# Kernel tuning notes

Hardware: AMD Instinct MI355X
Metric: run time of the kernel (lower is better)

The kernel has to match this reference:

```python
import jax, jax.numpy as jnp
import numpy as np

EMBED_DIM = 1024
N_HEADS = 16
HEAD_DIM = EMBED_DIM // N_HEADS


def setup_inputs() -> dict:
    key = jax.random.key(0)
    k_x, k_wi, k_bi, k_wo, k_bo = jax.random.split(key, 5)
    B, N, C = 4, 2048, EMBED_DIM
    scale = 1.0 / np.sqrt(C)
    return {
        "x": jax.random.normal(k_x, (B, N, C), dtype=jnp.float32),
        "w_in": jax.random.normal(k_wi, (C, 3 * C), dtype=jnp.float32) * scale,
        "b_in": jax.random.normal(k_bi, (3 * C,), dtype=jnp.float32) * 0.01,
        "w_out": jax.random.normal(k_wo, (C, C), dtype=jnp.float32) * scale,
        "b_out": jax.random.normal(k_bo, (C,), dtype=jnp.float32) * 0.01,
    }


def reference(x, w_in, b_in, w_out, b_out):
    B, N, C = x.shape
    H, D = N_HEADS, HEAD_DIM
    qkv = x @ w_in + b_in  # (B, N, 3C)
    q, k, v = jnp.split(qkv, 3, axis=-1)
    # (B, H, N, D)
    q = q.reshape(B, N, H, D).transpose(0, 2, 1, 3)
    k = k.reshape(B, N, H, D).transpose(0, 2, 1, 3)
    v = v.reshape(B, N, H, D).transpose(0, 2, 1, 3)
    # Naive attention: full (B,H,N,N) scores, NO sqrt(d) scaling (as in source)
    scores = jnp.einsum("bhnd,bhmd->bhnm", q, k)
    attn = jax.nn.softmax(scores, axis=-1)
    out = jnp.einsum("bhnm,bhmd->bhnd", attn, v)
    out = out.transpose(0, 2, 1, 3).reshape(B, N, C)
    return out @ w_out + b_out
```

## Files before the change

kernel.cpp:

```cpp
#include <hip/hip_runtime.h>
#include <hip/hip_bf16.h>
#include <stdint.h>

typedef __attribute__((ext_vector_type(8))) __bf16 bf8v;
typedef __attribute__((ext_vector_type(4))) float f4v;

#define L2E 1.44269504088896f

__device__ __forceinline__ unsigned short f2bf(float f) {
  union { float f; unsigned u; } v; v.f = f;
  unsigned r = v.u + 0x7fffu + ((v.u >> 16) & 1u);
  return (unsigned short)(r >> 16);
}

__device__ __forceinline__ unsigned pk2bf(float f0, float f1) {
  union { __hip_bfloat162 h; unsigned u; } c;
  c.h = __float22bfloat162_rn(make_float2(f0, f1));
  return c.u;
}

__device__ __forceinline__ float exp2_hw(float x) {
  return __builtin_amdgcn_exp2f(x);
}

__device__ __forceinline__ void gl_lds16(const void* g, void* l) {
  __builtin_amdgcn_global_load_lds(
      (__attribute__((address_space(1))) void*)(g),
      (__attribute__((address_space(3))) void*)(l), 16, 0, 0);
}

__global__ void cast_bf16_kernel(const float* __restrict__ in,
                                 unsigned short* __restrict__ out) {
  int i = blockIdx.x * 256 + threadIdx.x;
  float4 v = ((const float4*)in)[i];
  ushort4 o;
  o.x = f2bf(v.x); o.y = f2bf(v.y); o.z = f2bf(v.z); o.w = f2bf(v.w);
  ((ushort4*)out)[i] = o;
}

__global__ void transpose_w_kernel(const float* __restrict__ w_in,
                                   const float* __restrict__ w_out,
                                   unsigned short* __restrict__ wiT,
                                   unsigned short* __restrict__ woT) {
  __shared__ float tile[32][33];
  int bx = blockIdx.x;
  const float* in; unsigned short* out; int C, c0;
  if (bx < 96) { in = w_in;  out = wiT; C = 3072; c0 = bx * 32; }
  else         { in = w_out; out = woT; C = 1024; c0 = (bx - 96) * 32; }
  int r0 = blockIdx.y * 32;
  int tx = threadIdx.x, ty = threadIdx.y;
#pragma unroll
  for (int j = 0; j < 4; ++j)
    tile[ty + 8 * j][tx] = in[(size_t)(r0 + ty + 8 * j) * C + c0 + tx];
  __syncthreads();
#pragma unroll
  for (int j = 0; j < 4; ++j)
    out[(size_t)(c0 + ty + 8 * j) * 1024 + r0 + tx] = f2bf(tile[tx][ty + 8 * j]);
}

__global__ void transpose_v_kernel(const unsigned short* __restrict__ qkv,
                                   unsigned short* __restrict__ vtg) {
  __shared__ unsigned short tile[32][33];
  int bh = blockIdx.z;
  int d0 = blockIdx.y * 32;
  int n0 = blockIdx.x * 32;
  int b = bh >> 4, h = bh & 15;
  int tx = threadIdx.x, ty = threadIdx.y;
  const unsigned short* src = qkv + (size_t)b * 2048 * 3072 + 2048 + h * 64 + d0;
#pragma unroll
  for (int j = 0; j < 4; ++j)
    tile[ty + 8 * j][tx] = src[(size_t)(n0 + ty + 8 * j) * 3072 + tx];
  __syncthreads();
  unsigned short* dst = vtg + ((size_t)bh * 64) * 2048;
#pragma unroll
  for (int j = 0; j < 4; ++j)
    dst[(size_t)(d0 + ty + 8 * j) * 2048 + n0 + tx] = tile[tx][ty + 8 * j];
}

__global__ __launch_bounds__(256, 2) void gemm_bt(
    const unsigned short* __restrict__ A,
    const unsigned short* __restrict__ BT,
    const float* __restrict__ bias,
    unsigned short* __restrict__ C,
    int M, int N, int K, int scale_ncols, float scale) {
  __shared__ __align__(16) unsigned short As[128 * 32];
  __shared__ __align__(16) unsigned short Bs[128 * 32];
  const int tid = threadIdx.x;
  const int wave = tid >> 6, lane = tid & 63;
  const int lo = lane & 15, hi = lane >> 4;
  const int m0 = blockIdx.y * 128, n0 = blockIdx.x * 128;
  const int wm = (wave >> 1) * 64, wn = (wave & 1) * 64;

  f4v acc[4][4] = {};

  const int srow = lane >> 2;
  const int scol = (lane & 3) * 8;

  for (int k0 = 0; k0 < K; k0 += 32) {
#pragma unroll
    for (int p = 0; p < 2; ++p) {
      int r = p * 64 + wave * 16 + srow;
      gl_lds16(A + (size_t)(m0 + r) * K + k0 + scol,
               &As[(p * 64 + wave * 16) * 32]);
      gl_lds16(BT + (size_t)(n0 + r) * K + k0 + scol,
               &Bs[(p * 64 + wave * 16) * 32]);
    }
    __syncthreads();
    bf8v a[4], b[4];
#pragma unroll
    for (int i = 0; i < 4; ++i)
      a[i] = *(const bf8v*)&As[(wm + i * 16 + lo) * 32 + hi * 8];
#pragma unroll
    for (int j = 0; j < 4; ++j)
      b[j] = *(const bf8v*)&Bs[(wn + j * 16 + lo) * 32 + hi * 8];
#pragma unroll
    for (int i = 0; i < 4; ++i)
#pragma unroll
      for (int j = 0; j < 4; ++j)
        acc[i][j] = __builtin_amdgcn_mfma_f32_16x16x32_bf16(a[i], b[j], acc[i][j], 0, 0, 0);
    __syncthreads();
  }

#pragma unroll
  for (int i = 0; i < 4; ++i) {
#pragma unroll
    for (int r = 0; r < 4; ++r) {
      int row = m0 + wm + i * 16 + hi * 4 + r;
#pragma unroll
      for (int j = 0; j < 4; ++j) {
        int col = n0 + wn + j * 16 + lo;
        float v = acc[i][j][r] + bias[col];
        if (col < scale_ncols) v *= scale;
        C[(size_t)row * N + col] = f2bf(v);
      }
    }
  }
}

__global__ __launch_bounds__(256, 4) void gemm_bt_sm(
    const unsigned short* __restrict__ A,
    const unsigned short* __restrict__ BT,
    const float* __restrict__ bias,
    float* __restrict__ C,
    int M, int N, int K) {
  __shared__ __align__(16) unsigned short As[64 * 32];
  __shared__ __align__(16) unsigned short Bs[128 * 32];
  const int tid = threadIdx.x;
  const int wave = tid >> 6, lane = tid & 63;
  const int lo = lane & 15, hi = lane >> 4;
  const int m0 = blockIdx.y * 64, n0 = blockIdx.x * 128;
  const int wm = (wave >> 1) * 32, wn = (wave & 1) * 64;

  f4v acc[2][4] = {};

  const int srow = lane >> 2;
  const int scol = (lane & 3) * 8;

  for (int k0 = 0; k0 < K; k0 += 32) {
    gl_lds16(A + (size_t)(m0 + wave * 16 + srow) * K + k0 + scol,
             &As[(wave * 16) * 32]);
#pragma unroll
    for (int p = 0; p < 2; ++p) {
      int r = p * 64 + wave * 16 + srow;
      gl_lds16(BT + (size_t)(n0 + r) * K + k0 + scol,
               &Bs[(p * 64 + wave * 16) * 32]);
    }
    __syncthreads();
    bf8v a[2], b[4];
#pragma unroll
    for (int i = 0; i < 2; ++i)
      a[i] = *(const bf8v*)&As[(wm + i * 16 + lo) * 32 + hi * 8];
#pragma unroll
    for (int j = 0; j < 4; ++j)
      b[j] = *(const bf8v*)&Bs[(wn + j * 16 + lo) * 32 + hi * 8];
#pragma unroll
    for (int i = 0; i < 2; ++i)
#pragma unroll
      for (int j = 0; j < 4; ++j)
        acc[i][j] = __builtin_amdgcn_mfma_f32_16x16x32_bf16(a[i], b[j], acc[i][j], 0, 0, 0);
    __syncthreads();
  }

#pragma unroll
  for (int i = 0; i < 2; ++i) {
#pragma unroll
    for (int r = 0; r < 4; ++r) {
      int row = m0 + wm + i * 16 + hi * 4 + r;
#pragma unroll
      for (int j = 0; j < 4; ++j) {
        int col = n0 + wn + j * 16 + lo;
        C[(size_t)row * N + col] = acc[i][j][r] + bias[col];
      }
    }
  }
}

#define FSTR 72

__global__ __launch_bounds__(256, 4) void flash_attn(
    const unsigned short* __restrict__ qkv,
    const unsigned short* __restrict__ vtg,
    unsigned short* __restrict__ y) {
  __shared__ __align__(16) unsigned short Ps[128 * FSTR];
  __shared__ __align__(16) unsigned short Kt[64 * FSTR];
  __shared__ __align__(16) unsigned short Vt[64 * FSTR];
  const int tid = threadIdx.x;
  const int wave = tid >> 6, lane = tid & 63;
  const int lo = lane & 15, hi = lane >> 4;

  const int lin = (((blockIdx.z << 4) | blockIdx.y) << 4) | blockIdx.x;
  const int swz = (lin & 7) * 128 + (lin >> 3);
  const int q0 = (swz & 15) << 7;
  const int h  = (swz >> 4) & 15;
  const int b  = swz >> 8;

  const size_t base = (size_t)b * 2048 * 3072;
  const int qoff = h * 64, koff = 1024 + h * 64;
  const unsigned short* vsrc = vtg + (size_t)(b * 16 + h) * 64 * 2048;

  const int m_st = tid >> 3, c_st = tid & 7;
  const unsigned short* kg = qkv + base + koff;
  float4 rk0, rk1, rv0, rv1;
  auto kv_load = [&](int kt) {
    const int mb = kt * 64;
    rk0 = *(const float4*)(kg + (size_t)(mb + m_st) * 3072 + c_st * 8);
    rk1 = *(const float4*)(kg + (size_t)(mb + m_st + 32) * 3072 + c_st * 8);
    rv0 = *(const float4*)(vsrc + (size_t)m_st * 2048 + mb + c_st * 8);
    rv1 = *(const float4*)(vsrc + (size_t)(m_st + 32) * 2048 + mb + c_st * 8);
  };
  auto kv_write = [&]() {
    *(float4*)&Kt[m_st * FSTR + c_st * 8] = rk0;
    *(float4*)&Kt[(m_st + 32) * FSTR + c_st * 8] = rk1;
    *(float4*)&Vt[m_st * FSTR + c_st * 8] = rv0;
    *(float4*)&Vt[(m_st + 32) * FSTR + c_st * 8] = rv1;
  };

  kv_load(0);

#pragma unroll
  for (int i = 0; i < 4; ++i) {
    int cid = i * 256 + tid;
    int m = cid >> 3, c = cid & 7;
    *(float4*)&Ps[m * FSTR + c * 8] =
        *(const float4*)(qkv + base + (size_t)(q0 + m) * 3072 + qoff + c * 8);
  }
  __syncthreads();
  bf8v bq[2][2];
#pragma unroll
  for (int qt = 0; qt < 2; ++qt)
#pragma unroll
    for (int ks = 0; ks < 2; ++ks)
      bq[qt][ks] = *(const bf8v*)&Ps[(wave * 32 + qt * 16 + lo) * FSTR + ks * 32 + hi * 8];

  f4v O[2][4] = {};
  f4v acc_l[2] = {};
  union { bf8v v; unsigned short u[8]; } onesu;
#pragma unroll
  for (int i = 0; i < 8; ++i) onesu.u[i] = 0x3F80;
  const bf8v ones = onesu.v;

  for (int kt = 0; kt < 32; ++kt) {
    asm volatile("" ::: "memory");
    __builtin_amdgcn_s_barrier();
    asm volatile("" ::: "memory");
    kv_write();
    if (kt < 31) kv_load(kt + 1);
    asm volatile("s_waitcnt lgkmcnt(0)" ::: "memory");
    __builtin_amdgcn_s_barrier();
    asm volatile("" ::: "memory");

#pragma unroll
    for (int ct = 0; ct < 4; ++ct) {
      f4v s0 = {}, s1 = {};
      __builtin_amdgcn_s_setprio(1);
#pragma unroll
      for (int ks = 0; ks < 2; ++ks) {
        bf8v ak = *(const bf8v*)&Kt[(ct * 16 + lo) * FSTR + ks * 32 + hi * 8];
        s0 = __builtin_amdgcn_mfma_f32_16x16x32_bf16(ak, bq[0][ks], s0, 0, 0, 0);
        s1 = __builtin_amdgcn_mfma_f32_16x16x32_bf16(ak, bq[1][ks], s1, 0, 0, 0);
      }
      __builtin_amdgcn_s_setprio(0);
      {
        float p0 = exp2_hw(s0[0]), p1 = exp2_hw(s0[1]);
        float p2 = exp2_hw(s0[2]), p3 = exp2_hw(s0[3]);
        uint2 w; w.x = pk2bf(p0, p1); w.y = pk2bf(p2, p3);
        *(uint2*)&Ps[(wave * 32 + lo) * FSTR + ct * 16 + hi * 4] = w;
      }
      {
        float p0 = exp2_hw(s1[0]), p1 = exp2_hw(s1[1]);
        float p2 = exp2_hw(s1[2]), p3 = exp2_hw(s1[3]);
        uint2 w; w.x = pk2bf(p0, p1); w.y = pk2bf(p2, p3);
        *(uint2*)&Ps[(wave * 32 + 16 + lo) * FSTR + ct * 16 + hi * 4] = w;
      }
    }

#pragma unroll
    for (int ks = 0; ks < 2; ++ks) {
      bf8v ap0 = *(const bf8v*)&Ps[(wave * 32 + lo) * FSTR + ks * 32 + hi * 8];
      bf8v ap1 = *(const bf8v*)&Ps[(wave * 32 + 16 + lo) * FSTR + ks * 32 + hi * 8];
      __builtin_amdgcn_s_setprio(1);
      acc_l[0] = __builtin_amdgcn_mfma_f32_16x16x32_bf16(ap0, ones, acc_l[0], 0, 0, 0);
      acc_l[1] = __builtin_amdgcn_mfma_f32_16x16x32_bf16(ap1, ones, acc_l[1], 0, 0, 0);
#pragma unroll
      for (int dt = 0; dt < 4; ++dt) {
        bf8v bv = *(const bf8v*)&Vt[(dt * 16 + lo) * FSTR + ks * 32 + hi * 8];
        O[0][dt] = __builtin_amdgcn_mfma_f32_16x16x32_bf16(ap0, bv, O[0][dt], 0, 0, 0);
        O[1][dt] = __builtin_amdgcn_mfma_f32_16x16x32_bf16(ap1, bv, O[1][dt], 0, 0, 0);
      }
      __builtin_amdgcn_s_setprio(0);
    }
  }

#pragma unroll
  for (int qt = 0; qt < 2; ++qt) {
#pragma unroll
    for (int r = 0; r < 4; ++r) {
      float inv = 1.f / acc_l[qt][r];
      int row = q0 + wave * 32 + qt * 16 + hi * 4 + r;
      size_t orow = ((size_t)b * 2048 + row) * 1024 + h * 64;
#pragma unroll
      for (int dt = 0; dt < 4; ++dt)
        y[orow + dt * 16 + lo] = f2bf(O[qt][dt][r] * inv);
    }
  }
}

extern "C" void kernel_launch(void* const* d_in, const int* in_sizes, int n_in,
                              void* d_out, int out_size, void* d_ws, size_t ws_size,
                              hipStream_t stream) {
  (void)in_sizes; (void)n_in; (void)out_size; (void)ws_size;
  const float* x     = (const float*)d_in[0];
  const float* w_in  = (const float*)d_in[1];
  const float* b_in  = (const float*)d_in[2];
  const float* w_out = (const float*)d_in[3];
  const float* b_out = (const float*)d_in[4];

  unsigned short* xb  = (unsigned short*)d_ws;
  unsigned short* wiT = xb  + (size_t)8192 * 1024;
  unsigned short* woT = wiT + (size_t)3072 * 1024;
  unsigned short* qkv = woT + (size_t)1024 * 1024;
  unsigned short* yb  = qkv + (size_t)8192 * 3072;
  unsigned short* vtg = xb;

  cast_bf16_kernel<<<8192, 256, 0, stream>>>(x, xb);
  transpose_w_kernel<<<dim3(128, 32), dim3(32, 8), 0, stream>>>(w_in, w_out, wiT, woT);

  gemm_bt<<<dim3(24, 64), 256, 0, stream>>>(xb, wiT, b_in, qkv, 8192, 3072, 1024,
                                            1024, L2E);
  transpose_v_kernel<<<dim3(64, 2, 64), dim3(32, 8), 0, stream>>>(qkv, vtg);
  flash_attn<<<dim3(16, 16, 4), 256, 0, stream>>>(qkv, vtg, yb);
  gemm_bt_sm<<<dim3(8, 128), 256, 0, stream>>>(yb, woT, b_out, (float*)d_out,
                                               8192, 1024, 1024);
}
```

Baseline: 303.8 us.

## Rewrite QKV GEMM with 256x256 tiles, double-buffered LDS, swizzle and XCD remap

```diff
diff --git a/kernel.cpp b/kernel.cpp
--- a/kernel.cpp
+++ b/kernel.cpp
@@ -77,58 +77,99 @@
     dst[(size_t)(d0 + ty + 8 * j) * 2048 + n0 + tx] = tile[tx][ty + 8 * j];
 }
 
-__global__ __launch_bounds__(256, 2) void gemm_bt(
+__global__ __launch_bounds__(512, 2) void gemm_bt256(
     const unsigned short* __restrict__ A,
     const unsigned short* __restrict__ BT,
     const float* __restrict__ bias,
     unsigned short* __restrict__ C,
-    int M, int N, int K, int scale_ncols, float scale) {
-  __shared__ __align__(16) unsigned short As[128 * 32];
-  __shared__ __align__(16) unsigned short Bs[128 * 32];
+    int N, int K, int nbx, int scale_ncols, float scale) {
+  __shared__ __align__(16) unsigned short As[2][256 * 64];
+  __shared__ __align__(16) unsigned short Bs[2][256 * 64];
   const int tid = threadIdx.x;
   const int wave = tid >> 6, lane = tid & 63;
   const int lo = lane & 15, hi = lane >> 4;
-  const int m0 = blockIdx.y * 128, n0 = blockIdx.x * 128;
-  const int wm = (wave >> 1) * 64, wn = (wave & 1) * 64;
-
-  f4v acc[4][4] = {};
-
-  const int srow = lane >> 2;
-  const int scol = (lane & 3) * 8;
-
-  for (int k0 = 0; k0 < K; k0 += 32) {
-#pragma unroll
-    for (int p = 0; p < 2; ++p) {
-      int r = p * 64 + wave * 16 + srow;
-      gl_lds16(A + (size_t)(m0 + r) * K + k0 + scol,
-               &As[(p * 64 + wave * 16) * 32]);
-      gl_lds16(BT + (size_t)(n0 + r) * K + k0 + scol,
-               &Bs[(p * 64 + wave * 16) * 32]);
-    }
-    __syncthreads();
-    bf8v a[4], b[4];
-#pragma unroll
-    for (int i = 0; i < 4; ++i)
-      a[i] = *(const bf8v*)&As[(wm + i * 16 + lo) * 32 + hi * 8];
-#pragma unroll
-    for (int j = 0; j < 4; ++j)
-      b[j] = *(const bf8v*)&Bs[(wn + j * 16 + lo) * 32 + hi * 8];
-#pragma unroll
-    for (int i = 0; i < 4; ++i)
-#pragma unroll
-      for (int j = 0; j < 4; ++j)
-        acc[i][j] = __builtin_amdgcn_mfma_f32_16x16x32_bf16(a[i], b[j], acc[i][j], 0, 0, 0);
-    __syncthreads();
-  }
-
-#pragma unroll
-  for (int i = 0; i < 4; ++i) {
+  const int wm = wave >> 2, wn = wave & 3;
+
+  const int nwg = gridDim.x;
+  const int cpx = nwg >> 3;
+  const int s = (blockIdx.x & 7) * cpx + (blockIdx.x >> 3);
+  const int by = s / nbx, bx = s - by * nbx;
+  const int m0 = by * 256, n0 = bx * 256;
+
+  const int srow = lane >> 3;
+  const int scol = ((lane & 7) * 8) ^ ((lane >> 1) & 16);
+  const unsigned short* gA = A + (size_t)(m0 + wave * 8 + srow) * K + scol;
+  const unsigned short* gB = BT + (size_t)(n0 + wave * 8 + srow) * K + scol;
+
+  const int colsw0 = (hi * 8) ^ ((lo & 4) << 2);
+  const int colsw1 = (32 + hi * 8) ^ ((lo & 4) << 2);
+  const int rA = wm * 128 + lo;
+  const int rB = wn * 64 + lo;
+
+  f4v acc[8][4] = {};
+  const int nt = K >> 6;
+
+#pragma unroll
+  for (int j = 0; j < 4; ++j) {
+    gl_lds16(gA + (size_t)(j * 64) * K, &As[0][(j * 64 + wave * 8) * 64]);
+    gl_lds16(gB + (size_t)(j * 64) * K, &Bs[0][(j * 64 + wave * 8) * 64]);
+  }
+
+  for (int t = 0; t < nt; ++t) {
+    const int c = t & 1;
+    __builtin_amdgcn_s_barrier();
+    __builtin_amdgcn_sched_barrier(0);
+    if (t + 1 < nt) {
+      const unsigned short* gA1 = gA + (size_t)(t + 1) * 64;
+      const unsigned short* gB1 = gB + (size_t)(t + 1) * 64;
+#pragma unroll
+      for (int j = 0; j < 4; ++j) {
+        gl_lds16(gA1 + (size_t)(j * 64) * K, &As[c ^ 1][(j * 64 + wave * 8) * 64]);
+        gl_lds16(gB1 + (size_t)(j * 64) * K, &Bs[c ^ 1][(j * 64 + wave * 8) * 64]);
+      }
+      asm volatile("s_waitcnt vmcnt(8)" ::: "memory");
+    } else {
+      asm volatile("s_waitcnt vmcnt(0)" ::: "memory");
+    }
+    __builtin_amdgcn_sched_barrier(0);
+    __builtin_amdgcn_s_barrier();
+    __builtin_amdgcn_sched_barrier(0);
+
+    bf8v b[4][2];
+#pragma unroll
+    for (int fn = 0; fn < 4; ++fn) {
+      b[fn][0] = *(const bf8v*)&Bs[c][(rB + fn * 16) * 64 + colsw0];
+      b[fn][1] = *(const bf8v*)&Bs[c][(rB + fn * 16) * 64 + colsw1];
+    }
+#pragma unroll
+    for (int p = 0; p < 4; ++p) {
+      bf8v a[2][2];
+#pragma unroll
+      for (int i = 0; i < 2; ++i) {
+        a[i][0] = *(const bf8v*)&As[c][(rA + (p * 2 + i) * 16) * 64 + colsw0];
+        a[i][1] = *(const bf8v*)&As[c][(rA + (p * 2 + i) * 16) * 64 + colsw1];
+      }
+      __builtin_amdgcn_s_setprio(1);
+#pragma unroll
+      for (int ks = 0; ks < 2; ++ks)
+#pragma unroll
+        for (int i = 0; i < 2; ++i)
+#pragma unroll
+          for (int fn = 0; fn < 4; ++fn)
+            acc[p * 2 + i][fn] = __builtin_amdgcn_mfma_f32_16x16x32_bf16(
+                a[i][ks], b[fn][ks], acc[p * 2 + i][fn], 0, 0, 0);
+      __builtin_amdgcn_s_setprio(0);
+    }
+  }
+
+#pragma unroll
+  for (int i = 0; i < 8; ++i) {
 #pragma unroll
     for (int r = 0; r < 4; ++r) {
-      int row = m0 + wm + i * 16 + hi * 4 + r;
+      int row = m0 + wm * 128 + i * 16 + hi * 4 + r;
 #pragma unroll
       for (int j = 0; j < 4; ++j) {
-        int col = n0 + wn + j * 16 + lo;
+        int col = n0 + wn * 64 + j * 16 + lo;
         float v = acc[i][j][r] + bias[col];
         if (col < scale_ncols) v *= scale;
         C[(size_t)row * N + col] = f2bf(v);
@@ -345,8 +386,7 @@
   cast_bf16_kernel<<<8192, 256, 0, stream>>>(x, xb);
   transpose_w_kernel<<<dim3(128, 32), dim3(32, 8), 0, stream>>>(w_in, w_out, wiT, woT);
 
-  gemm_bt<<<dim3(24, 64), 256, 0, stream>>>(xb, wiT, b_in, qkv, 8192, 3072, 1024,
-                                            1024, L2E);
+  gemm_bt256<<<384, 512, 0, stream>>>(xb, wiT, b_in, qkv, 3072, 1024, 12, 1024, L2E);
   transpose_v_kernel<<<dim3(64, 2, 64), dim3(32, 8), 0, stream>>>(qkv, vtg);
   flash_attn<<<dim3(16, 16, 4), 256, 0, stream>>>(qkv, vtg, yb);
   gemm_bt_sm<<<dim3(8, 128), 256, 0, stream>>>(yb, woT, b_out, (float*)d_out,
```

Result: no change. 303.2 us (-0.2%).
